# Optimization experiments

Measured on AMD Instinct MI355X. Metric: run time of the kernel, lower is better.

The kernel has to match this reference:

```python
import jax, jax.numpy as jnp
import numpy as np

B, T, K = 512, 1024, 48

def setup_inputs() -> dict:
    key = jax.random.key(0)
    k_em, k_tag, k_len, k_tr, k_st, k_en = jax.random.split(key, 6)
    emissions = jax.random.normal(k_em, (B, T, K), dtype=jnp.float32)
    tags = jax.random.randint(k_tag, (B, T), 0, K)
    lengths = jax.random.randint(k_len, (B,), T // 2, T + 1)
    mask = jnp.arange(T)[None, :] < lengths[:, None]  # [B, T] bool, left-contiguous, mask[:,0]=True
    transitions = jax.random.uniform(k_tr, (K, K), minval=-0.1, maxval=0.1, dtype=jnp.float32)
    start_transitions = jax.random.uniform(k_st, (K,), minval=-0.1, maxval=0.1, dtype=jnp.float32)
    end_transitions = jax.random.uniform(k_en, (K,), minval=-0.1, maxval=0.1, dtype=jnp.float32)
    return {"emissions": emissions, "tags": tags, "mask": mask,
            "transitions": transitions, "start_transitions": start_transitions,
            "end_transitions": end_transitions}

def _crf_log_likelihood(emissions, transitions, start_transitions, end_transitions, tags, mask):
    b_idx = jnp.arange(emissions.shape[0])
    maskf = mask.astype(emissions.dtype)
    # ---- numerator: score of gold path ----
    emit_scores = jnp.take_along_axis(emissions, tags[:, :, None], axis=2)[:, :, 0]  # [B, T]
    trans_scores = transitions[tags[:, :-1], tags[:, 1:]]  # [B, T-1], trans[prev, cur]
    score = start_transitions[tags[:, 0]] + emit_scores[:, 0]
    score = score + jnp.sum((emit_scores[:, 1:] + trans_scores) * maskf[:, 1:], axis=1)
    last_idx = jnp.sum(mask, axis=1).astype(jnp.int32) - 1
    score = score + end_transitions[tags[b_idx, last_idx]]
    # ---- denominator: log partition via forward algorithm ----
    # NOTE: faithful to source, which indexes transitions[cur, prev] here (transposed vs numerator)
    alpha0 = start_transitions[None, :] + emissions[:, 0]  # [B, K]
    es = jnp.swapaxes(emissions[:, 1:], 0, 1)  # [T-1, B, K]
    ms = jnp.swapaxes(mask[:, 1:], 0, 1)       # [T-1, B]
    def step(alpha, xm):
        e_t, m_t = xm
        # next[b, x] = LSE_y(alpha[b, y] + trans[x, y]) + e_t[b, x]
        nxt = jax.nn.logsumexp(alpha[:, None, :] + transitions[None, :, :], axis=2) + e_t
        alpha = jnp.where(m_t[:, None], nxt, alpha)
        return alpha, None
    alpha, _ = jax.lax.scan(step, alpha0, (es, ms))
    log_den = jax.nn.logsumexp(alpha + end_transitions[None, :], axis=1)  # [B]
    return score - log_den

def reference(emissions, tags, mask, transitions, start_transitions, end_transitions):
    return _crf_log_likelihood(emissions, transitions, start_transitions, end_transitions, tags, mask)
```

## Files before the change

kernel.cpp:

```cpp
#include <hip/hip_runtime.h>
#include <math.h>

#define BB 512
#define TT 1024
#define KK 48
#define SEG 17
#define CENTER 6

typedef _Float16 f16x8 __attribute__((ext_vector_type(8)));
typedef _Float16 f16x4 __attribute__((ext_vector_type(4)));
typedef float    f32x4 __attribute__((ext_vector_type(4)));

#if __has_builtin(__builtin_amdgcn_mfma_f32_16x16x16f16)
#define HAVE_X16 1
#else
#define HAVE_X16 0
#endif

static constexpr float L2E = 1.4426950408889634f;
static constexpr float LN2 = 0.6931471805599453f;

__device__ __forceinline__ float wave_reduce_sum_f(float v) {
    #pragma unroll
    for (int m = 32; m >= 1; m >>= 1) v += __shfl_xor(v, m, 64);
    return v;
}
__device__ __forceinline__ int wave_reduce_sum_i(int v) {
    #pragma unroll
    for (int m = 32; m >= 1; m >>= 1) v += __shfl_xor(v, m, 64);
    return v;
}

__device__ __forceinline__ int count_L(const void* mask, int b, int lane, unsigned w0) {
    int c = 0;
    if (w0 == 1u) {
        const int* mp = (const int*)mask + (size_t)b * TT;
        for (int t = lane; t < TT; t += 64) c += (mp[t] != 0);
    } else if (w0 == 0x3f800000u) {
        const float* mp = (const float*)mask + (size_t)b * TT;
        for (int t = lane; t < TT; t += 64) c += (mp[t] != 0.0f);
    } else {
        const unsigned char* mp = (const unsigned char*)mask + (size_t)b * TT;
        for (int t = lane; t < TT; t += 64) c += (mp[t] != 0);
    }
    return wave_reduce_sum_i(c);
}

__device__ __forceinline__ f32x4 mfma32(f16x8 a, f16x8 b, f32x4 c) {
    return __builtin_amdgcn_mfma_f32_16x16x32_f16(a, b, c, 0, 0, 0);
}

__device__ __forceinline__ float max12(const f32x4* v) {
    float mx = 0.0f;
    #pragma unroll
    for (int m = 0; m < 3; ++m) {
        #pragma unroll
        for (int e = 0; e < 4; ++e) mx = fmaxf(mx, v[m][e]);
    }
    return mx;
}

template <int BWD>
__device__ void scan_mfma(
    const float* __restrict__ em, const float* __restrict__ transitions,
    const float* __restrict__ start_t, const float* __restrict__ end_t,
    int Lb, int lane, float (*sh_V)[KK], float* sh_D)
{
    const int c = lane & 15;
    const int g = lane >> 4;
    const int i = BWD ? (c + 1) : c;
    const int N = Lb - 1;
    const int base = N / SEG, rem = N % SEG;
    const bool extra = (i < rem);
    const int len  = base + (extra ? 1 : 0);
    const int a    = 1 + i * base + (extra ? i : rem);

    f16x8 A0[3];
    #pragma unroll
    for (int r = 0; r < 3; ++r) {
        f16x8 fr;
        #pragma unroll
        for (int e = 0; e < 8; ++e) {
            const int k = 16 * (e >> 2) + 4 * g + (e & 3);
            const int j = 16 * r + c;
            fr[e] = (_Float16)exp2f((BWD ? transitions[k * KK + j]
                                         : transitions[j * KK + k]) * L2E);
        }
        A0[r] = fr;
    }
#if HAVE_X16
    f16x4 A1[3];
    #pragma unroll
    for (int r = 0; r < 3; ++r) {
        f16x4 fr;
        #pragma unroll
        for (int e = 0; e < 4; ++e) {
            const int k = 32 + 4 * g + e;
            const int j = 16 * r + c;
            fr[e] = (_Float16)exp2f((BWD ? transitions[k * KK + j]
                                         : transitions[j * KK + k]) * L2E);
        }
        A1[r] = fr;
    }
#else
    f16x8 A1[3];
    #pragma unroll
    for (int r = 0; r < 3; ++r) {
        f16x8 fr;
        #pragma unroll
        for (int e = 0; e < 8; ++e) {
            const int k = 32 + 16 * (e >> 2) + 4 * g + (e & 3);
            const int j = 16 * r + c;
            float tv = 0.0f;
            if (k < KK)
                tv = exp2f((BWD ? transitions[k * KK + j]
                                : transitions[j * KK + k]) * L2E);
            fr[e] = (_Float16)tv;
        }
        A1[r] = fr;
    }
#endif

    const int t0 = a + len - 1;
    const float* pe = em + (size_t)(BWD ? t0 : a) * KK + 4 * g;
    const int pstep = BWD ? -KK : KK;

    f32x4 braw[3];
    #pragma unroll
    for (int m = 0; m < 3; ++m) {
        f32x4 bv;
        #pragma unroll
        for (int e = 0; e < 4; ++e) {
            const int k = 16 * m + 4 * g + e;
            float u0;
            if (BWD) u0 = (c == 15) ? exp2f(end_t[k] * L2E) : 1.0f;
            else     u0 = (c == 0) ? exp2f((start_t[k] + em[k]) * L2E) : 1.0f;
            bv[e] = u0;
        }
        braw[m] = bv;
    }
    if (BWD) {
        #pragma unroll
        for (int m = 0; m < 3; ++m) {
            const f32x4 ev = *(const f32x4*)(pe + 16 * m);
            #pragma unroll
            for (int e = 0; e < 4; ++e) braw[m][e] *= exp2f(ev[e] * L2E);
        }
        pe += pstep;
    }

    f32x4 cur[3], nxt[3];
    #pragma unroll
    for (int m = 0; m < 3; ++m) cur[m] = *(const f32x4*)(pe + 16 * m);
    pe += pstep;

    int D = 0, Dprev = 0;
    float mx = max12(braw);
    mx = fmaxf(mx, __shfl_xor(mx, 16));
    mx = fmaxf(mx, __shfl_xor(mx, 32));
    int dadj = (int)((__float_as_uint(mx) >> 23) & 0xFF) - 127 + CENTER;

    f16x8 B0;
#if HAVE_X16
    f16x4 B1;
#else
    f16x8 B1;
#endif
    {
        B0 = (f16x8){(_Float16)braw[0][0], (_Float16)braw[0][1],
                     (_Float16)braw[0][2], (_Float16)braw[0][3],
                     (_Float16)braw[1][0], (_Float16)braw[1][1],
                     (_Float16)braw[1][2], (_Float16)braw[1][3]};
#if HAVE_X16
        B1 = (f16x4){(_Float16)braw[2][0], (_Float16)braw[2][1],
                     (_Float16)braw[2][2], (_Float16)braw[2][3]};
#else
        B1 = (f16x8){(_Float16)braw[2][0], (_Float16)braw[2][1],
                     (_Float16)braw[2][2], (_Float16)braw[2][3],
                     (_Float16)0, (_Float16)0, (_Float16)0, (_Float16)0};
#endif
    }

    f32x4 C[3];

    #pragma unroll 1
    for (int s = 1; s <= base; ++s) {
        #pragma unroll
        for (int m = 0; m < 3; ++m) nxt[m] = *(const f32x4*)(pe + 16 * m);
        pe += pstep;

        #pragma unroll
        for (int r = 0; r < 3; ++r) {
            f32x4 z = {0.0f, 0.0f, 0.0f, 0.0f};
            z = mfma32(A0[r], B0, z);
#if HAVE_X16
            z = __builtin_amdgcn_mfma_f32_16x16x16f16(A1[r], B1, z, 0, 0, 0);
#else
            z = mfma32(A1[r], B1, z);
#endif
            C[r] = z;
        }

        const float nd = -(float)dadj;
        #pragma unroll
        for (int m = 0; m < 3; ++m) {
            #pragma unroll
            for (int e = 0; e < 4; ++e)
                braw[m][e] = C[m][e] * exp2f(fmaf(cur[m][e], L2E, nd));
        }
        Dprev = D;
        D += dadj;
        float mx2 = max12(braw);
        mx2 = fmaxf(mx2, __shfl_xor(mx2, 16));
        mx2 = fmaxf(mx2, __shfl_xor(mx2, 32));
        dadj = (int)((__float_as_uint(mx2) >> 23) & 0xFF) - 127 + CENTER;

        B0 = (f16x8){(_Float16)braw[0][0], (_Float16)braw[0][1],
                     (_Float16)braw[0][2], (_Float16)braw[0][3],
                     (_Float16)braw[1][0], (_Float16)braw[1][1],
                     (_Float16)braw[1][2], (_Float16)braw[1][3]};
#if HAVE_X16
        B1 = (f16x4){(_Float16)braw[2][0], (_Float16)braw[2][1],
                     (_Float16)braw[2][2], (_Float16)braw[2][3]};
#else
        B1 = (f16x8){(_Float16)braw[2][0], (_Float16)braw[2][1],
                     (_Float16)braw[2][2], (_Float16)braw[2][3],
                     (_Float16)0, (_Float16)0, (_Float16)0, (_Float16)0};
#endif

        #pragma unroll
        for (int m = 0; m < 3; ++m) cur[m] = nxt[m];
    }

    #pragma unroll
    for (int r = 0; r < 3; ++r) {
        #pragma unroll
        for (int e = 0; e < 4; ++e)
            sh_V[c][16 * r + 4 * g + e] = BWD ? C[r][e] : braw[r][e];
    }
    if (g == 0) sh_D[c] = (float)(BWD ? Dprev : D);

    #pragma unroll
    for (int r = 0; r < 3; ++r) {
        f32x4 z = {0.0f, 0.0f, 0.0f, 0.0f};
        z = mfma32(A0[r], B0, z);
#if HAVE_X16
        z = __builtin_amdgcn_mfma_f32_16x16x16f16(A1[r], B1, z, 0, 0, 0);
#else
        z = mfma32(A1[r], B1, z);
#endif
        C[r] = z;
    }
    float Dx;
    if (BWD) {
        Dx = (float)D;
    } else {
        const float nd = -(float)dadj;
        #pragma unroll
        for (int m = 0; m < 3; ++m) {
            #pragma unroll
            for (int e = 0; e < 4; ++e)
                C[m][e] = C[m][e] * exp2f(fmaf(cur[m][e], L2E, nd));
        }
        Dx = (float)(D + dadj);
    }
    if (extra) {
        #pragma unroll
        for (int r = 0; r < 3; ++r) {
            #pragma unroll
            for (int e = 0; e < 4; ++e)
                sh_V[c][16 * r + 4 * g + e] = C[r][e];
        }
        if (g == 0) sh_D[c] = Dx;
    }
}

__global__ __launch_bounds__(192, 1) void crf_all(
    const float* __restrict__ emissions,
    const int*   __restrict__ tags,
    const void*  __restrict__ mask,
    const float* __restrict__ transitions,
    const float* __restrict__ start_t,
    const float* __restrict__ end_t,
    float*       __restrict__ out)
{
    const int b    = blockIdx.x;
    const int wid  = threadIdx.x >> 6;
    const int lane = threadIdx.x & 63;
    __shared__ float sh_F[16][KK];
    __shared__ float sh_G[16][KK];
    __shared__ float sh_DF[16];
    __shared__ float sh_DG[16];
    __shared__ float sh_sc;

    const unsigned w0 = *((const unsigned*)mask);
    const int L = count_L(mask, b, lane, w0);
    const float* em = emissions + (size_t)b * TT * KK;

    if (wid == 0) {
        scan_mfma<0>(em, transitions, start_t, end_t, L, lane, sh_F, sh_DF);
    } else if (wid == 1) {
        scan_mfma<1>(em, transitions, start_t, end_t, L, lane, sh_G, sh_DG);
    } else {
        const int* tg = tags + (size_t)b * TT;
        float sc = 0.0f;
        for (int t = lane; t < TT; t += 64) {
            if (t < L) {
                const int tagt = tg[t];
                float term = em[(size_t)t * KK + tagt];
                term += (t == 0) ? start_t[tagt] : transitions[tg[t - 1] * KK + tagt];
                sc += term;
            }
        }
        sc = wave_reduce_sum_f(sc);
        if (lane == 0) sh_sc = sc + end_t[tg[L - 1]];
    }
    __syncthreads();

    if (wid == 0) {
        const int k = lane >> 2;
        const int q = lane & 3;
        float dot = 0.0f, ns = 0.0f;
        #pragma unroll
        for (int e = 0; e < 12; ++e) {
            const int j = q * 12 + e;
            const float f = sh_F[k][j];
            dot += sh_G[k][j] * f;
            ns  += f;
        }
        dot += __shfl_xor(dot, 1, 64); dot += __shfl_xor(dot, 2, 64);
        ns  += __shfl_xor(ns, 1, 64);  ns  += __shfl_xor(ns, 2, 64);
        float v = 0.0f;
        if (q == 0) {
            v = log2f(dot) + sh_DG[k];
            if (k >= 1) v -= log2f(ns);
        }
        const float acc = wave_reduce_sum_f(v);
        if (lane == 0) out[b] = sh_sc - LN2 * (acc + sh_DF[0]);
    }
}

extern "C" void kernel_launch(void* const* d_in, const int* in_sizes, int n_in,
                              void* d_out, int out_size, void* d_ws, size_t ws_size,
                              hipStream_t stream) {
    const float* emissions   = (const float*)d_in[0];
    const int*   tags        = (const int*)  d_in[1];
    const void*  mask        = (const void*) d_in[2];
    const float* transitions = (const float*)d_in[3];
    const float* start_t     = (const float*)d_in[4];
    const float* end_t       = (const float*)d_in[5];
    float* out = (float*)d_out;
    (void)d_ws; (void)ws_size;

    crf_all<<<BB, 192, 0, stream>>>(emissions, tags, mask, transitions,
                                    start_t, end_t, out);
}
```

Baseline: 186.7 us.

## Double scan segments to 33 with two waves per direction and deeper emission prefetch

Raises the number of time segments from 17 to 33 so the forward and backward scans each use two waves (16 segments per wave), which roughly halves the serial chain length per lane. The block grows from 192 to 320 threads. The single-step emission lookahead becomes a 4-deep register prefetch ring with a tail loop, to hide global load latency on the serial dependency chain. The combine step now reduces 32 segment boundaries. The cost is more waves per block, more registers for the prefetch buffers, and extra combine work.

```diff
diff --git a/kernel.cpp b/kernel.cpp
--- a/kernel.cpp
+++ b/kernel.cpp
@@ -4,7 +4,8 @@
 #define BB 512
 #define TT 1024
 #define KK 48
-#define SEG 17
+#define SEG 33
+#define PF 4
 #define CENTER 6
 
 typedef _Float16 f16x8 __attribute__((ext_vector_type(8)));
@@ -64,16 +65,17 @@
 __device__ void scan_mfma(
     const float* __restrict__ em, const float* __restrict__ transitions,
     const float* __restrict__ start_t, const float* __restrict__ end_t,
-    int Lb, int lane, float (*sh_V)[KK], float* sh_D)
+    int Lb, int lane, int wofs, float (*sh_V)[KK], float* sh_D)
 {
     const int c = lane & 15;
     const int g = lane >> 4;
-    const int i = BWD ? (c + 1) : c;
+    const int i = wofs + c + (BWD ? 1 : 0);
     const int N = Lb - 1;
     const int base = N / SEG, rem = N % SEG;
     const bool extra = (i < rem);
     const int len  = base + (extra ? 1 : 0);
     const int a    = 1 + i * base + (extra ? i : rem);
+    const int t0   = a + len - 1;
 
     f16x8 A0[3];
     #pragma unroll
@@ -121,10 +123,6 @@
     }
 #endif
 
-    const int t0 = a + len - 1;
-    const float* pe = em + (size_t)(BWD ? t0 : a) * KK + 4 * g;
-    const int pstep = BWD ? -KK : KK;
-
     f32x4 braw[3];
     #pragma unroll
     for (int m = 0; m < 3; ++m) {
@@ -133,26 +131,31 @@
         for (int e = 0; e < 4; ++e) {
             const int k = 16 * m + 4 * g + e;
             float u0;
-            if (BWD) u0 = (c == 15) ? exp2f(end_t[k] * L2E) : 1.0f;
-            else     u0 = (c == 0) ? exp2f((start_t[k] + em[k]) * L2E) : 1.0f;
+            if (BWD) u0 = (i == SEG - 1) ? exp2f(end_t[k] * L2E) : 1.0f;
+            else     u0 = (i == 0) ? exp2f((start_t[k] + em[k]) * L2E) : 1.0f;
             bv[e] = u0;
         }
         braw[m] = bv;
     }
     if (BWD) {
+        const float* p0 = em + (size_t)t0 * KK + 4 * g;
         #pragma unroll
         for (int m = 0; m < 3; ++m) {
-            const f32x4 ev = *(const f32x4*)(pe + 16 * m);
+            const f32x4 ev = *(const f32x4*)(p0 + 16 * m);
             #pragma unroll
             for (int e = 0; e < 4; ++e) braw[m][e] *= exp2f(ev[e] * L2E);
         }
-        pe += pstep;
-    }
-
-    f32x4 cur[3], nxt[3];
-    #pragma unroll
-    for (int m = 0; m < 3; ++m) cur[m] = *(const f32x4*)(pe + 16 * m);
-    pe += pstep;
+    }
+
+    f32x4 buf[PF][3];
+    #pragma unroll
+    for (int k = 0; k < PF; ++k) {
+        int t = BWD ? (t0 - 1 - k) : (a + k);
+        t = t < 0 ? 0 : (t > TT - 1 ? TT - 1 : t);
+        const float* p = em + (size_t)t * KK + 4 * g;
+        #pragma unroll
+        for (int m = 0; m < 3; ++m) buf[k][m] = *(const f32x4*)(p + 16 * m);
+    }
 
     int D = 0, Dprev = 0;
     float mx = max12(braw);
@@ -166,29 +169,22 @@
 #else
     f16x8 B1;
 #endif
-    {
-        B0 = (f16x8){(_Float16)braw[0][0], (_Float16)braw[0][1],
-                     (_Float16)braw[0][2], (_Float16)braw[0][3],
-                     (_Float16)braw[1][0], (_Float16)braw[1][1],
-                     (_Float16)braw[1][2], (_Float16)braw[1][3]};
-#if HAVE_X16
-        B1 = (f16x4){(_Float16)braw[2][0], (_Float16)braw[2][1],
-                     (_Float16)braw[2][2], (_Float16)braw[2][3]};
-#else
-        B1 = (f16x8){(_Float16)braw[2][0], (_Float16)braw[2][1],
-                     (_Float16)braw[2][2], (_Float16)braw[2][3],
-                     (_Float16)0, (_Float16)0, (_Float16)0, (_Float16)0};
-#endif
-    }
+    B0 = (f16x8){(_Float16)braw[0][0], (_Float16)braw[0][1],
+                 (_Float16)braw[0][2], (_Float16)braw[0][3],
+                 (_Float16)braw[1][0], (_Float16)braw[1][1],
+                 (_Float16)braw[1][2], (_Float16)braw[1][3]};
+#if HAVE_X16
+    B1 = (f16x4){(_Float16)braw[2][0], (_Float16)braw[2][1],
+                 (_Float16)braw[2][2], (_Float16)braw[2][3]};
+#else
+    B1 = (f16x8){(_Float16)braw[2][0], (_Float16)braw[2][1],
+                 (_Float16)braw[2][2], (_Float16)braw[2][3],
+                 (_Float16)0, (_Float16)0, (_Float16)0, (_Float16)0};
+#endif
 
     f32x4 C[3];
 
-    #pragma unroll 1
-    for (int s = 1; s <= base; ++s) {
-        #pragma unroll
-        for (int m = 0; m < 3; ++m) nxt[m] = *(const f32x4*)(pe + 16 * m);
-        pe += pstep;
-
+    auto STEP = [&](const f32x4* E) {
         #pragma unroll
         for (int r = 0; r < 3; ++r) {
             f32x4 z = {0.0f, 0.0f, 0.0f, 0.0f};
@@ -200,13 +196,12 @@
 #endif
             C[r] = z;
         }
-
         const float nd = -(float)dadj;
         #pragma unroll
         for (int m = 0; m < 3; ++m) {
             #pragma unroll
             for (int e = 0; e < 4; ++e)
-                braw[m][e] = C[m][e] * exp2f(fmaf(cur[m][e], L2E, nd));
+                braw[m][e] = C[m][e] * exp2f(fmaf(E[m][e], L2E, nd));
         }
         Dprev = D;
         D += dadj;
@@ -214,7 +209,6 @@
         mx2 = fmaxf(mx2, __shfl_xor(mx2, 16));
         mx2 = fmaxf(mx2, __shfl_xor(mx2, 32));
         dadj = (int)((__float_as_uint(mx2) >> 23) & 0xFF) - 127 + CENTER;
-
         B0 = (f16x8){(_Float16)braw[0][0], (_Float16)braw[0][1],
                      (_Float16)braw[0][2], (_Float16)braw[0][3],
                      (_Float16)braw[1][0], (_Float16)braw[1][1],
@@ -227,19 +221,44 @@
                      (_Float16)braw[2][2], (_Float16)braw[2][3],
                      (_Float16)0, (_Float16)0, (_Float16)0, (_Float16)0};
 #endif
-
-        #pragma unroll
-        for (int m = 0; m < 3; ++m) cur[m] = nxt[m];
-    }
-
+    };
+
+    int sb = 1;
+    int tn = BWD ? (t0 - 1 - PF) : (a + PF);
+    #pragma unroll 1
+    for (; sb + PF - 1 <= base; sb += PF) {
+        #pragma unroll
+        for (int k = 0; k < PF; ++k) {
+            STEP(buf[k]);
+            int t = tn + (BWD ? -k : k);
+            t = t < 0 ? 0 : (t > TT - 1 ? TT - 1 : t);
+            const float* p = em + (size_t)t * KK + 4 * g;
+            #pragma unroll
+            for (int m = 0; m < 3; ++m) buf[k][m] = *(const f32x4*)(p + 16 * m);
+        }
+        tn += BWD ? -PF : PF;
+    }
+    const int lsteps = base - sb + 1;
+    #pragma unroll
+    for (int k = 0; k < PF - 1; ++k)
+        if (k < lsteps) STEP(buf[k]);
+
+    const int slot = wofs + c;
     #pragma unroll
     for (int r = 0; r < 3; ++r) {
         #pragma unroll
         for (int e = 0; e < 4; ++e)
-            sh_V[c][16 * r + 4 * g + e] = BWD ? C[r][e] : braw[r][e];
-    }
-    if (g == 0) sh_D[c] = (float)(BWD ? Dprev : D);
-
+            sh_V[slot][16 * r + 4 * g + e] = BWD ? C[r][e] : braw[r][e];
+    }
+    if (g == 0) sh_D[slot] = (float)(BWD ? Dprev : D);
+
+    f32x4 epE[3];
+    #pragma unroll
+    for (int k = 0; k < PF; ++k) {
+        if (k == lsteps) {
+            epE[0] = buf[k][0]; epE[1] = buf[k][1]; epE[2] = buf[k][2];
+        }
+    }
     #pragma unroll
     for (int r = 0; r < 3; ++r) {
         f32x4 z = {0.0f, 0.0f, 0.0f, 0.0f};
@@ -260,7 +279,7 @@
         for (int m = 0; m < 3; ++m) {
             #pragma unroll
             for (int e = 0; e < 4; ++e)
-                C[m][e] = C[m][e] * exp2f(fmaf(cur[m][e], L2E, nd));
+                C[m][e] = C[m][e] * exp2f(fmaf(epE[m][e], L2E, nd));
         }
         Dx = (float)(D + dadj);
     }
@@ -269,13 +288,13 @@
         for (int r = 0; r < 3; ++r) {
             #pragma unroll
             for (int e = 0; e < 4; ++e)
-                sh_V[c][16 * r + 4 * g + e] = C[r][e];
-        }
-        if (g == 0) sh_D[c] = Dx;
-    }
-}
-
-__global__ __launch_bounds__(192, 1) void crf_all(
+                sh_V[slot][16 * r + 4 * g + e] = C[r][e];
+        }
+        if (g == 0) sh_D[slot] = Dx;
+    }
+}
+
+__global__ __launch_bounds__(320, 1) void crf_all(
     const float* __restrict__ emissions,
     const int*   __restrict__ tags,
     const void*  __restrict__ mask,
@@ -287,20 +306,20 @@
     const int b    = blockIdx.x;
     const int wid  = threadIdx.x >> 6;
     const int lane = threadIdx.x & 63;
-    __shared__ float sh_F[16][KK];
-    __shared__ float sh_G[16][KK];
-    __shared__ float sh_DF[16];
-    __shared__ float sh_DG[16];
+    __shared__ float sh_F[SEG - 1][KK];
+    __shared__ float sh_G[SEG - 1][KK];
+    __shared__ float sh_DF[SEG - 1];
+    __shared__ float sh_DG[SEG - 1];
     __shared__ float sh_sc;
 
     const unsigned w0 = *((const unsigned*)mask);
     const int L = count_L(mask, b, lane, w0);
     const float* em = emissions + (size_t)b * TT * KK;
 
-    if (wid == 0) {
-        scan_mfma<0>(em, transitions, start_t, end_t, L, lane, sh_F, sh_DF);
-    } else if (wid == 1) {
-        scan_mfma<1>(em, transitions, start_t, end_t, L, lane, sh_G, sh_DG);
+    if (wid < 2) {
+        scan_mfma<0>(em, transitions, start_t, end_t, L, lane, wid * 16, sh_F, sh_DF);
+    } else if (wid < 4) {
+        scan_mfma<1>(em, transitions, start_t, end_t, L, lane, (wid - 2) * 16, sh_G, sh_DG);
     } else {
         const int* tg = tags + (size_t)b * TT;
         float sc = 0.0f;
@@ -318,18 +337,18 @@
     __syncthreads();
 
     if (wid == 0) {
-        const int k = lane >> 2;
-        const int q = lane & 3;
+        const int k = lane >> 1;
+        const int q = lane & 1;
         float dot = 0.0f, ns = 0.0f;
         #pragma unroll
-        for (int e = 0; e < 12; ++e) {
-            const int j = q * 12 + e;
+        for (int e = 0; e < 24; ++e) {
+            const int j = q * 24 + e;
             const float f = sh_F[k][j];
             dot += sh_G[k][j] * f;
             ns  += f;
         }
-        dot += __shfl_xor(dot, 1, 64); dot += __shfl_xor(dot, 2, 64);
-        ns  += __shfl_xor(ns, 1, 64);  ns  += __shfl_xor(ns, 2, 64);
+        dot += __shfl_xor(dot, 1, 64);
+        ns  += __shfl_xor(ns, 1, 64);
         float v = 0.0f;
         if (q == 0) {
             v = log2f(dot) + sh_DG[k];
@@ -352,6 +371,6 @@
     float* out = (float*)d_out;
     (void)d_ws; (void)ws_size;
 
-    crf_all<<<BB, 192, 0, stream>>>(emissions, tags, mask, transitions,
+    crf_all<<<BB, 320, 0, stream>>>(emissions, tags, mask, transitions,
                                     start_t, end_t, out);
 }
```

Result: faster. 172.0 us (-7.9%).
